# Optimization experiments

Hardware: AMD Instinct MI355X
Metric: run time of the kernel (lower is better)

The kernel has to match this reference:

```python
import jax, jax.numpy as jnp
import numpy as np

BATCH, SEQ, D_MODEL, STATE_DIM = 8, 2048, 1024, 1024


def setup_inputs() -> dict:
    key = jax.random.key(0)
    k1, k2, k3, k4 = jax.random.split(key, 4)
    u = jax.random.normal(k1, (BATCH, SEQ, D_MODEL), dtype=jnp.float32)
    a_params = jax.random.normal(k2, (STATE_DIM // 2,), dtype=jnp.float32) * 0.1
    # nn.Linear default init ~ U(-1/sqrt(fan_in), 1/sqrt(fan_in)); scaled normal is fine for a baseline
    B_w = jax.random.normal(k3, (STATE_DIM, D_MODEL), dtype=jnp.float32) / np.sqrt(D_MODEL).astype(np.float32)
    C_w = jax.random.normal(k4, (D_MODEL, STATE_DIM), dtype=jnp.float32) / np.sqrt(STATE_DIM).astype(np.float32)
    D = jnp.zeros((D_MODEL,), dtype=jnp.float32)
    return {"u": u, "a_params": a_params, "B_w": B_w, "C_w": C_w, "D": D}


def _cayley_circulant_eigenvalues(a_params, n):
    # Build skew-circulant first column: a[0]=0, a[1:n/2]=a_params[:n/2-1], a[n/2]=0,
    # a[n/2+1:] = -flip(a_params[:n/2-1]); eigenvalues are purely imaginary: i*omega.
    half_n = n // 2
    a_full = jnp.zeros((n,), dtype=a_params.dtype)
    a_full = a_full.at[1:half_n].set(a_params[: half_n - 1])
    a_full = a_full.at[half_n + 1 :].set(-a_params[: half_n - 1][::-1])
    omega = jnp.fft.fft(a_full).imag
    # Cayley transform (1 - i*w)/(1 + i*w) = ((1-w^2) - 2iw) / (1+w^2)
    w2 = omega * omega
    denom = 1.0 + w2
    return (((1.0 - w2) / denom) + 1j * (-2.0 * omega / denom)).astype(jnp.complex64)


def reference(u, a_params, B_w, C_w, D):
    n = B_w.shape[0]
    lambdas = _cayley_circulant_eigenvalues(a_params, n)  # (n,) complex64
    Bu = jnp.einsum("bsd,nd->bsn", u, B_w)  # (b, s, n)

    def step(h, bu_t):
        # W h via FFT diagonalization of the circulant W (W real => real part exact)
        Wh = jnp.fft.ifft(lambdas * jnp.fft.fft(h.astype(jnp.float32))).real.astype(h.dtype)
        h_new = Wh + bu_t
        return h_new, h_new

    h0 = jnp.zeros((u.shape[0], n), dtype=u.dtype)
    _, hs = jax.lax.scan(step, h0, jnp.swapaxes(Bu, 0, 1))  # hs: (s, b, n)
    y = jnp.einsum("sbn,dn->bsd", hs, C_w) + D * u  # (b, s, d)
    return y
```

## Files before the change

kernel.cpp:

```cpp
#include <hip/hip_runtime.h>
#include <math.h>

#define BATCH   8
#define SEQLEN  2048
#define DMODEL  1024
#define KFREQ   513
#define NSPEC   1024
#define NPAIR   512
#define BT_ROWS (BATCH*SEQLEN)
#define NC      32
#define TC      64

static_assert(NC * TC == SEQLEN, "chunking must cover SEQLEN");

typedef __attribute__((ext_vector_type(4))) float f32x4;
typedef __attribute__((ext_vector_type(8))) short bf16x8;
typedef unsigned short ushort_t;
typedef unsigned int uint_t;

__device__ __forceinline__ ushort_t f2bf(float f) {
    union { float f; unsigned u; } v; v.f = f;
    unsigned r = v.u + 0x7FFFu + ((v.u >> 16) & 1u);
    return (ushort_t)(r >> 16);
}
__device__ __forceinline__ float bf2f(ushort_t b) {
    union { unsigned u; float f; } v; v.u = ((unsigned)b) << 16;
    return v.f;
}

__device__ __forceinline__ void async_cp16(const void* g, void* l) {
    __builtin_amdgcn_global_load_lds(
        (const __attribute__((address_space(1))) void*)g,
        (__attribute__((address_space(3))) void*)l, 16, 0, 0);
}

#define BAR()   __builtin_amdgcn_s_barrier()
#define PRIO1() __builtin_amdgcn_s_setprio(1)
#define PRIO0() __builtin_amdgcn_s_setprio(0)
#define LGKM0() asm volatile("s_waitcnt lgkmcnt(0)" ::: "memory")
#define LGKM8() asm volatile("s_waitcnt lgkmcnt(8)" ::: "memory")
#define VM6()   asm volatile("s_waitcnt vmcnt(6)" ::: "memory")
#define VM0()   asm volatile("s_waitcnt vmcnt(0)" ::: "memory")

#define SINSTEP 0.00613592315154256491887f

#define NB_T  (NSPEC * DMODEL / 8 / 256)
#define NB_TR 256
#define NB_CW (DMODEL * DMODEL / 8 / 256)
#define NB_U  (BT_ROWS * DMODEL / 8 / 256)

__global__ __launch_bounds__(256) void prep_all(const float* __restrict__ ap,
                                                float* __restrict__ lam,
                                                const float* __restrict__ Dv,
                                                int* __restrict__ dflag,
                                                const float* __restrict__ Cw,
                                                ushort_t* __restrict__ Cwb,
                                                const float* __restrict__ Bw,
                                                ushort_t* __restrict__ BwTb,
                                                ushort_t* __restrict__ T1b,
                                                ushort_t* __restrict__ T2b,
                                                const float* __restrict__ u,
                                                ushort_t* __restrict__ ub) {
    const int bid = blockIdx.x;
    if (bid == 0) {
        __shared__ float stab[1024];
        __shared__ float apl[512];
        __shared__ int anyd;
        if (threadIdx.x == 0) anyd = 0;
        for (int j = threadIdx.x; j < 1024; j += 256)
            stab[j] = sinf((float)j * SINSTEP);
        for (int j = threadIdx.x; j < 511; j += 256)
            apl[j] = ap[j];
        __syncthreads();
        for (int q = threadIdx.x; q < 1024; q += 256)
            if (Dv[q] != 0.0f) anyd = 1;
        for (int f = threadIdx.x; f < KFREQ; f += 256) {
            float o0 = 0.0f, o1 = 0.0f, o2 = 0.0f, o3 = 0.0f;
            int j = 1;
            for (; j + 3 <= 511; j += 4) {
                o0 = fmaf(apl[j - 1], stab[(j * f) & 1023], o0);
                o1 = fmaf(apl[j],     stab[((j + 1) * f) & 1023], o1);
                o2 = fmaf(apl[j + 1], stab[((j + 2) * f) & 1023], o2);
                o3 = fmaf(apl[j + 2], stab[((j + 3) * f) & 1023], o3);
            }
            for (; j <= 511; ++j)
                o0 = fmaf(apl[j - 1], stab[(j * f) & 1023], o0);
            const float om = ((o0 + o1) + (o2 + o3)) * -2.0f;
            const float w2 = om * om;
            const float den = 1.0f + w2;
            const float re = (1.0f - w2) / den;
            const float im = -2.0f * om / den;
            if (f == 0)        lam[0] = re;
            else if (f == 512) lam[1] = re;
            else { lam[2 * f] = re; lam[2 * f + 1] = im; }
        }
        __syncthreads();
        if (threadIdx.x == 0) *dflag = anyd;
    } else if (bid < 1 + 2 * NB_T) {
        __shared__ float stab[1024];
        for (int j = threadIdx.x; j < 1024; j += 256)
            stab[j] = sinf((float)j * SINSTEP);
        __syncthreads();
        const int t = bid - 1;
        const int mode = t >= NB_T;
        ushort_t* T = mode ? T2b : T1b;
        const int i = (t - mode * NB_T) * 256 + threadIdx.x;
        const int row = i >> 7;
        const int nb  = (i & 127) << 3;
        const int kf  = (row == 1) ? 512 : (row >> 1);
        const bool sb = (row & 1) && (row != 1);
        float scale = 1.0f;
        if (mode) scale = ((row < 2) ? 1.0f : 2.0f) / 1024.0f;
        ushort_t o[8];
        int m = (kf * nb) & 1023;
#pragma unroll
        for (int j = 0; j < 8; ++j) {
            const float v = sb ? -stab[m] : stab[(m + 256) & 1023];
            o[j] = f2bf(v * scale);
            m = (m + kf) & 1023;
        }
        reinterpret_cast<bf16x8*>(T)[i] = *reinterpret_cast<bf16x8*>(o);
    } else if (bid < 1 + 2 * NB_T + NB_TR) {
        __shared__ float tile[64][65];
        const int b2 = bid - (1 + 2 * NB_T);
        const int bx = (b2 & 15) * 64;
        const int by = (b2 >> 4) * 64;
        const int lx = threadIdx.x & 63;
        const int ly = threadIdx.x >> 6;
#pragma unroll
        for (int i = 0; i < 16; ++i) {
            const int r = ly + i * 4;
            tile[r][lx] = Bw[(size_t)(by + r) * DMODEL + bx + lx];
        }
        __syncthreads();
#pragma unroll
        for (int i = 0; i < 16; ++i) {
            const int r = ly + i * 4;
            BwTb[(size_t)(bx + r) * DMODEL + by + lx] = f2bf(tile[lx][r]);
        }
    } else if (bid < 1 + 2 * NB_T + NB_TR + NB_CW) {
        const int b3 = bid - (1 + 2 * NB_T + NB_TR);
        const int i = b3 * 256 + threadIdx.x;
        const float4 a = reinterpret_cast<const float4*>(Cw)[2 * i];
        const float4 b = reinterpret_cast<const float4*>(Cw)[2 * i + 1];
        ushort_t o[8] = {f2bf(a.x), f2bf(a.y), f2bf(a.z), f2bf(a.w),
                         f2bf(b.x), f2bf(b.y), f2bf(b.z), f2bf(b.w)};
        reinterpret_cast<bf16x8*>(Cwb)[i] = *reinterpret_cast<bf16x8*>(o);
    } else {
        const int b4 = bid - (1 + 2 * NB_T + NB_TR + NB_CW);
        const int i = b4 * 256 + threadIdx.x;
        const float4 a = reinterpret_cast<const float4*>(u)[2 * i];
        const float4 b = reinterpret_cast<const float4*>(u)[2 * i + 1];
        ushort_t o[8] = {f2bf(a.x), f2bf(a.y), f2bf(a.z), f2bf(a.w),
                         f2bf(b.x), f2bf(b.y), f2bf(b.z), f2bf(b.w)};
        reinterpret_cast<bf16x8*>(ub)[i] = *reinterpret_cast<bf16x8*>(o);
    }
}

__global__ __launch_bounds__(256) void gemm128z(const ushort_t* __restrict__ A0,
                                                const ushort_t* __restrict__ B0,
                                                ushort_t* __restrict__ C0,
                                                const ushort_t* __restrict__ A1,
                                                const ushort_t* __restrict__ B1,
                                                ushort_t* __restrict__ C1) {
    const int K = 1024, N = 1024;
    const ushort_t* A = blockIdx.z ? A1 : A0;
    const ushort_t* B = blockIdx.z ? B1 : B0;
    ushort_t*       C = blockIdx.z ? C1 : C0;
    __shared__ ushort_t As[128 * 32];
    __shared__ ushort_t Bs[128 * 32];
    const int tid  = threadIdx.x;
    const int lane = tid & 63;
    const int w    = tid >> 6;
    const int m0 = blockIdx.x * 128;
    const int n0 = blockIdx.y * 128;
    const int wr = (w >> 1) * 64;
    const int wc = (w & 1) * 64;

    f32x4 acc[4][4] = {};

    const int pos  = w * 512 + lane * 8;
    const int srow = pos >> 5;
    const int scol = pos & 31;
    const int lr = lane & 15;
    const int lk = (lane >> 4) * 8;

    for (int k0 = 0; k0 < K; k0 += 32) {
        __syncthreads();
        async_cp16(A + (size_t)(m0 + srow)      * K + k0 + scol, As + w * 512);
        async_cp16(A + (size_t)(m0 + srow + 64) * K + k0 + scol, As + 2048 + w * 512);
        async_cp16(B + (size_t)(n0 + srow)      * K + k0 + scol, Bs + w * 512);
        async_cp16(B + (size_t)(n0 + srow + 64) * K + k0 + scol, Bs + 2048 + w * 512);
        __syncthreads();

        bf16x8 fa[4], fb[4];
#pragma unroll
        for (int mi = 0; mi < 4; ++mi)
            fa[mi] = *reinterpret_cast<const bf16x8*>(&As[(wr + mi * 16 + lr) * 32 + lk]);
#pragma unroll
        for (int ni = 0; ni < 4; ++ni)
            fb[ni] = *reinterpret_cast<const bf16x8*>(&Bs[(wc + ni * 16 + lr) * 32 + lk]);
#pragma unroll
        for (int mi = 0; mi < 4; ++mi)
#pragma unroll
            for (int ni = 0; ni < 4; ++ni)
                acc[mi][ni] = __builtin_amdgcn_mfma_f32_16x16x32_bf16(
                    fa[mi], fb[ni], acc[mi][ni], 0, 0, 0);
    }

    const int rbase = (lane >> 4) * 4;
#pragma unroll
    for (int mi = 0; mi < 4; ++mi)
#pragma unroll
        for (int ni = 0; ni < 4; ++ni) {
            const int col = n0 + wc + ni * 16 + lr;
#pragma unroll
            for (int j = 0; j < 4; ++j) {
                const int row = m0 + wr + mi * 16 + rbase + j;
                C[(size_t)row * N + col] = f2bf(acc[mi][ni][j]);
            }
        }
}

__device__ __forceinline__ void pair_coef(const float* lam, int j,
                                          float& lr, float& lr2, float& cr) {
    const float a = lam[2 * j];
    const float b = lam[2 * j + 1];
    if (j == 0) { lr = a; lr2 = b; cr = 0.0f; }
    else        { lr = a; lr2 = a; cr = b; }
}

template <int MH, int NH>
__device__ __forceinline__ void quad_mfma(f32x4 (&acc)[2][2][4][2],
                                          const bf16x8 (&fa)[4][2],
                                          const bf16x8 (&fb)[2][2]) {
#pragma unroll
    for (int mi = 0; mi < 4; ++mi)
#pragma unroll
        for (int ni = 0; ni < 2; ++ni) {
            acc[MH][NH][mi][ni] = __builtin_amdgcn_mfma_f32_16x16x32_bf16(
                fa[mi][0], fb[ni][0], acc[MH][NH][mi][ni], 0, 0, 0);
            acc[MH][NH][mi][ni] = __builtin_amdgcn_mfma_f32_16x16x32_bf16(
                fa[mi][1], fb[ni][1], acc[MH][NH][mi][ni], 0, 0, 0);
        }
}

__device__ __forceinline__ void ld_fa(bf16x8 (&fa)[4][2], const ushort_t* hb,
                                      int wm, int lr, int c0, int c1) {
#pragma unroll
    for (int mi = 0; mi < 4; ++mi) {
        const ushort_t* p = hb + (wm * 64 + mi * 16 + lr) * 64;
        fa[mi][0] = *reinterpret_cast<const bf16x8*>(p + c0);
        fa[mi][1] = *reinterpret_cast<const bf16x8*>(p + c1);
    }
}
__device__ __forceinline__ void ld_fb(bf16x8 (&fb)[2][2], const ushort_t* hb,
                                      int wn, int lr, int c0, int c1) {
#pragma unroll
    for (int ni = 0; ni < 2; ++ni) {
        const ushort_t* p = hb + (wn * 32 + ni * 16 + lr) * 64;
        fb[ni][0] = *reinterpret_cast<const bf16x8*>(p + c0);
        fb[ni][1] = *reinterpret_cast<const bf16x8*>(p + c1);
    }
}

#define HS_STRIDE 260

template <bool SCANEPI>
__global__ __launch_bounds__(512, 2) void gemm256(const ushort_t* __restrict__ A,
                                                  const ushort_t* __restrict__ B,
                                                  void* __restrict__ Cv,
                                                  int M, int K,
                                                  const float* __restrict__ uu,
                                                  const float* __restrict__ Dv,
                                                  const int* __restrict__ dflag,
                                                  const float* __restrict__ lam,
                                                  float2* __restrict__ G) {
    __shared__ ushort_t smem[66560];
    const int tid  = threadIdx.x;
    const int lane = tid & 63;
    const int w    = tid >> 6;
    const int wm   = w >> 2;
    const int wn   = w & 3;
    const int m0 = blockIdx.x * 256;
    const int n0 = blockIdx.y * 256;
    const int lr = lane & 15;
    const int lk = (lane >> 4) * 8;
    const int xv = (lr & 7) << 3;
    const int c0 = lk ^ xv;
    const int c1 = (32 + lk) ^ xv;

    const int rA = tid >> 3;
    const int cS = ((tid & 7) << 3) ^ ((rA & 7) << 3);
    const int ldsOff = w << 9;

    auto ApH = [&](int buf, int half) { return smem + (buf * 2 + half) * 8192; };
    auto BpH = [&](int buf, int half) { return smem + 32768 + (buf * 2 + half) * 8192; };

    f32x4 acc[2][2][4][2] = {};
    bf16x8 fa[4][2], fbl[2][2], fbh[2][2];

    auto stA = [&](int buf, int half, int k) {
#pragma unroll
        for (int li = 0; li < 2; ++li)
            async_cp16(A + (size_t)(m0 + half * 128 + li * 64 + rA) * K + k + cS,
                       ApH(buf, half) + li * 4096 + ldsOff);
    };
    auto stB = [&](int buf, int half, int k) {
#pragma unroll
        for (int li = 0; li < 2; ++li)
            async_cp16(B + (size_t)(n0 + half * 128 + li * 64 + rA) * K + k + cS,
                       BpH(buf, half) + li * 4096 + ldsOff);
    };

    stA(0, 0, 0); stB(0, 0, 0); stB(0, 1, 0); stA(0, 1, 0);
    stA(1, 0, 64); stB(1, 0, 64); stB(1, 1, 64);
    VM6();
    BAR();

    const int niter = K >> 7;
#pragma unroll 1
    for (int t = 0; t < niter - 1; ++t) {
        const int kb1 = (t << 7) + 64;
        const int kn  = (t + 1) << 7;
        const int kn2 = kn + 64;
        ld_fa(fa, ApH(0, 0), wm, lr, c0, c1);
        ld_fb(fbl, BpH(0, 0), wn, lr, c0, c1);
        stA(1, 1, kb1);
        LGKM8();
        BAR(); LGKM0();
        PRIO1(); quad_mfma<0, 0>(acc, fa, fbl); PRIO0();
        BAR();
        ld_fb(fbh, BpH(0, 1), wn, lr, c0, c1);
        stA(0, 0, kn);
        BAR(); LGKM0();
        PRIO1(); quad_mfma<0, 1>(acc, fa, fbh); PRIO0();
        BAR();
        ld_fa(fa, ApH(0, 1), wm, lr, c0, c1);
        stB(0, 0, kn);
        BAR(); LGKM0();
        PRIO1(); quad_mfma<1, 1>(acc, fa, fbh); PRIO0();
        BAR();
        stB(0, 1, kn);
        VM6();
        BAR();
        PRIO1(); quad_mfma<1, 0>(acc, fa, fbl); PRIO0();
        BAR();
        ld_fa(fa, ApH(1, 0), wm, lr, c0, c1);
        ld_fb(fbl, BpH(1, 0), wn, lr, c0, c1);
        stA(0, 1, kn);
        LGKM8();
        BAR(); LGKM0();
        PRIO1(); quad_mfma<0, 0>(acc, fa, fbl); PRIO0();
        BAR();
        ld_fb(fbh, BpH(1, 1), wn, lr, c0, c1);
        stA(1, 0, kn2);
        BAR(); LGKM0();
        PRIO1(); quad_mfma<0, 1>(acc, fa, fbh); PRIO0();
        BAR();
        ld_fa(fa, ApH(1, 1), wm, lr, c0, c1);
        stB(1, 0, kn2);
        BAR(); LGKM0();
        PRIO1(); quad_mfma<1, 1>(acc, fa, fbh); PRIO0();
        BAR();
        stB(1, 1, kn2);
        VM6();
        BAR();
        PRIO1(); quad_mfma<1, 0>(acc, fa, fbl); PRIO0();
        BAR();
    }
    {
        const int kb1 = ((niter - 1) << 7) + 64;
        ld_fa(fa, ApH(0, 0), wm, lr, c0, c1);
        ld_fb(fbl, BpH(0, 0), wn, lr, c0, c1);
        stA(1, 1, kb1);
        LGKM8();
        BAR(); LGKM0();
        PRIO1(); quad_mfma<0, 0>(acc, fa, fbl); PRIO0();
        BAR();
        ld_fb(fbh, BpH(0, 1), wn, lr, c0, c1);
        BAR(); LGKM0();
        PRIO1(); quad_mfma<0, 1>(acc, fa, fbh); PRIO0();
        BAR();
        ld_fa(fa, ApH(0, 1), wm, lr, c0, c1);
        BAR(); LGKM0();
        PRIO1(); quad_mfma<1, 1>(acc, fa, fbh); PRIO0();
        BAR();
        VM0();
        BAR();
        PRIO1(); quad_mfma<1, 0>(acc, fa, fbl); PRIO0();
        BAR();
        ld_fa(fa, ApH(1, 0), wm, lr, c0, c1);
        ld_fb(fbl, BpH(1, 0), wn, lr, c0, c1);
        BAR(); LGKM0();
        PRIO1(); quad_mfma<0, 0>(acc, fa, fbl); PRIO0();
        BAR();
        ld_fb(fbh, BpH(1, 1), wn, lr, c0, c1);
        BAR(); LGKM0();
        PRIO1(); quad_mfma<0, 1>(acc, fa, fbh); PRIO0();
        BAR();
        ld_fa(fa, ApH(1, 1), wm, lr, c0, c1);
        BAR(); LGKM0();
        PRIO1(); quad_mfma<1, 1>(acc, fa, fbh); PRIO0();
        BAR();
        PRIO1(); quad_mfma<1, 0>(acc, fa, fbl); PRIO0();
    }

    const int rbase = (lane >> 4) * 4;
    if (SCANEPI) {
        BAR();
#pragma unroll
        for (int mh = 0; mh < 2; ++mh)
#pragma unroll
            for (int nh = 0; nh < 2; ++nh)
#pragma unroll
                for (int mi = 0; mi < 4; ++mi)
#pragma unroll
                    for (int ni = 0; ni < 2; ++ni) {
                        const int cl = nh * 128 + wn * 32 + ni * 16 + lr;
#pragma unroll
                        for (int j = 0; j < 4; ++j) {
                            const int rl = mh * 128 + wm * 64 + mi * 16 + rbase + j;
                            smem[rl * HS_STRIDE + cl] = f2bf(acc[mh][nh][mi][ni][j]);
                        }
                    }
        BAR();
        const int chunk = tid >> 7;
        const int p = tid & 127;
        const int jg = (n0 >> 1) + p;
        float lr_, lr2_, cr_;
        pair_coef(lam, jg, lr_, lr2_, cr_);
        uint_t* gout = reinterpret_cast<uint_t*>((ushort_t*)Cv +
                        (size_t)(m0 + chunk * TC) * NSPEC) + jg;
        float er = 0.0f, ei = 0.0f;
        for (int t = 0; t < TC; ++t) {
            const uint_t v = *reinterpret_cast<const uint_t*>(
                &smem[(chunk * TC + t) * HS_STRIDE + 2 * p]);
            const float ur = bf2f((ushort_t)(v & 0xFFFF));
            const float ui = bf2f((ushort_t)(v >> 16));
            const float nr = fmaf(lr_, er, fmaf(-cr_, ei, ur));
            const float ni = fmaf(lr2_, ei, fmaf(cr_, er, ui));
            gout[(size_t)t * NPAIR] = (uint_t)f2bf(nr) | ((uint_t)f2bf(ni) << 16);
            er = nr; ei = ni;
        }
        const int b = m0 >> 11;
        const int cg = ((m0 & 2047) >> 6) + chunk;
        G[(size_t)(b * NC + cg) * NPAIR + jg] = make_float2(er, ei);
    } else {
        float* C = (float*)Cv;
        const bool du = (*dflag != 0);
#pragma unroll
        for (int mh = 0; mh < 2; ++mh)
#pragma unroll
            for (int nh = 0; nh < 2; ++nh)
#pragma unroll
                for (int mi = 0; mi < 4; ++mi)
#pragma unroll
                    for (int ni = 0; ni < 2; ++ni) {
                        const int col = n0 + nh * 128 + wn * 32 + ni * 16 + lr;
#pragma unroll
                        for (int j = 0; j < 4; ++j) {
                            const int row = m0 + mh * 128 + wm * 64 + mi * 16 + rbase + j;
                            float v = acc[mh][nh][mi][ni][j];
                            if (du) v = fmaf(Dv[col], uu[(size_t)row * DMODEL + col], v);
                            C[(size_t)row * DMODEL + col] = v;
                        }
                    }
    }
}

__global__ __launch_bounds__(256) void scan_applyc(ushort_t* __restrict__ UHb,
                                                   const float* __restrict__ lam,
                                                   const float2* __restrict__ G) {
    const int gid = blockIdx.x * 256 + threadIdx.x;
    const int j = gid & (NPAIR - 1);
    const int s9 = gid >> 9;
    const int c = 1 + s9 % 31;
    const int b = s9 / 31;
    float lr, lr2, cr;
    pair_coef(lam, j, lr, lr2, cr);
    float pr = lr, pr2 = lr2, pc = cr;
    for (int s = 0; s < 6; ++s) {
        const float nr  = pr * pr - pc * pc;
        const float nr2 = pr2 * pr2 - pc * pc;
        const float npc = pc * (pr + pr2);
        pr = nr; pr2 = nr2; pc = npc;
    }
    float er = 0.0f, ei = 0.0f;
    for (int cp = 0; cp < c; ++cp) {
        const float2 g = G[(size_t)(b * NC + cp) * NPAIR + j];
        const float nr = fmaf(pr, er, fmaf(-pc, ei, g.x));
        const float ni = fmaf(pr2, ei, fmaf(pc, er, g.y));
        er = nr; ei = ni;
    }
    float sr = fmaf(lr, er, -cr * ei);
    float si = fmaf(lr2, ei, cr * er);
    uint_t* base = reinterpret_cast<uint_t*>(
        UHb + (size_t)(b * SEQLEN + c * TC) * NSPEC) + j;
    for (int t = 0; t < TC; ++t) {
        const uint_t v = base[(size_t)t * NPAIR];
        const float hr = bf2f((ushort_t)(v & 0xFFFF)) + sr;
        const float hi = bf2f((ushort_t)(v >> 16)) + si;
        base[(size_t)t * NPAIR] = (uint_t)f2bf(hr) | ((uint_t)f2bf(hi) << 16);
        const float nsr = fmaf(lr, sr, -cr * si);
        const float nsi = fmaf(lr2, si, cr * sr);
        sr = nsr; si = nsi;
    }
}

extern "C" void kernel_launch(void* const* d_in, const int* in_sizes, int n_in,
                              void* d_out, int out_size, void* d_ws, size_t ws_size,
                              hipStream_t stream) {
    const float* u  = (const float*)d_in[0];
    const float* ap = (const float*)d_in[1];
    const float* Bw = (const float*)d_in[2];
    const float* Cw = (const float*)d_in[3];
    const float* Dv = (const float*)d_in[4];
    float* out = (float*)d_out;

    char* ws = (char*)d_ws;
    size_t off = 0;
    auto carve = [&](size_t bytes) { char* p = ws + off; off += (bytes + 255) & ~(size_t)255; return p; };

    ushort_t* UHb  = (ushort_t*)carve((size_t)BT_ROWS * NSPEC * sizeof(ushort_t));
    ushort_t* ub   = (ushort_t*)carve((size_t)BT_ROWS * DMODEL * sizeof(ushort_t));
    ushort_t* T1b  = (ushort_t*)carve((size_t)NSPEC * DMODEL * sizeof(ushort_t));
    ushort_t* T2b  = (ushort_t*)carve((size_t)NSPEC * DMODEL * sizeof(ushort_t));
    ushort_t* BwTb = (ushort_t*)carve((size_t)DMODEL * DMODEL * sizeof(ushort_t));
    ushort_t* Cwb  = (ushort_t*)carve((size_t)DMODEL * DMODEL * sizeof(ushort_t));
    ushort_t* W1b  = (ushort_t*)carve((size_t)NSPEC * DMODEL * sizeof(ushort_t));
    ushort_t* W2b  = (ushort_t*)carve((size_t)DMODEL * NSPEC * sizeof(ushort_t));
    float*    lam  = (float*)   carve(NSPEC * sizeof(float));
    int*      dflag= (int*)     carve(sizeof(int));
    float2*   G    = (float2*)  carve((size_t)BATCH * NC * NPAIR * sizeof(float2));

    prep_all<<<1 + 2 * NB_T + NB_TR + NB_CW + NB_U, 256, 0, stream>>>(
        ap, lam, Dv, dflag, Cw, Cwb, Bw, BwTb, T1b, T2b, u, ub);

    {
        dim3 g(8, 8, 2);
        gemm128z<<<g, 256, 0, stream>>>(T1b, BwTb, W1b, Cwb, T2b, W2b);
    }

    {
        dim3 g(BT_ROWS / 256, NSPEC / 256);
        gemm256<true><<<g, 512, 0, stream>>>(ub, W1b, UHb,
            BT_ROWS, DMODEL, nullptr, nullptr, dflag, lam, G);
    }

    scan_applyc<<<BATCH * 31 * NPAIR / 256, 256, 0, stream>>>(UHb, lam, G);

    {
        dim3 g(BT_ROWS / 256, DMODEL / 256);
        gemm256<false><<<g, 512, 0, stream>>>(UHb, W2b, out,
            BT_ROWS, NSPEC, u, Dv, dflag, lam, nullptr);
    }
}
```

Before: 145.5 us.

## Fuse chunk-carry scan into first GEMM epilogue via grid-wide atomic barrier

Drops the separate scan_applyc kernel. The first GEMM now keeps its chunk-local scan results in LDS, publishes chunk carries to G, and waits at a grid-wide atomic counter barrier. It then combines the prefix carries and writes the corrected hidden states to global memory once, instead of writing them and later reading and rewriting them. The gain is one fewer launch and one fewer read-modify-write pass over UHb. The risk is deadlock if the 64x4=256 blocks are not all resident at once (2 per CU, 256 CUs), plus some idle time while blocks spin.

```diff
diff --git a/kernel.cpp b/kernel.cpp
--- a/kernel.cpp
+++ b/kernel.cpp
@@ -60,13 +60,14 @@
                                                 ushort_t* __restrict__ T1b,
                                                 ushort_t* __restrict__ T2b,
                                                 const float* __restrict__ u,
-                                                ushort_t* __restrict__ ub) {
+                                                ushort_t* __restrict__ ub,
+                                                uint_t* __restrict__ cnt) {
     const int bid = blockIdx.x;
     if (bid == 0) {
         __shared__ float stab[1024];
         __shared__ float apl[512];
         __shared__ int anyd;
-        if (threadIdx.x == 0) anyd = 0;
+        if (threadIdx.x == 0) { anyd = 0; *cnt = 0; }
         for (int j = threadIdx.x; j < 1024; j += 256)
             stab[j] = sinf((float)j * SINSTEP);
         for (int j = threadIdx.x; j < 511; j += 256)
@@ -275,7 +276,8 @@
                                                   const float* __restrict__ Dv,
                                                   const int* __restrict__ dflag,
                                                   const float* __restrict__ lam,
-                                                  float2* __restrict__ G) {
+                                                  float2* __restrict__ G,
+                                                  uint_t* __restrict__ cnt) {
     __shared__ ushort_t smem[66560];
     const int tid  = threadIdx.x;
     const int lane = tid & 63;
@@ -430,22 +432,65 @@
         const int jg = (n0 >> 1) + p;
         float lr_, lr2_, cr_;
         pair_coef(lam, jg, lr_, lr2_, cr_);
-        uint_t* gout = reinterpret_cast<uint_t*>((ushort_t*)Cv +
-                        (size_t)(m0 + chunk * TC) * NSPEC) + jg;
-        float er = 0.0f, ei = 0.0f;
-        for (int t = 0; t < TC; ++t) {
-            const uint_t v = *reinterpret_cast<const uint_t*>(
-                &smem[(chunk * TC + t) * HS_STRIDE + 2 * p]);
-            const float ur = bf2f((ushort_t)(v & 0xFFFF));
-            const float ui = bf2f((ushort_t)(v >> 16));
-            const float nr = fmaf(lr_, er, fmaf(-cr_, ei, ur));
-            const float ni = fmaf(lr2_, ei, fmaf(cr_, er, ui));
-            gout[(size_t)t * NPAIR] = (uint_t)f2bf(nr) | ((uint_t)f2bf(ni) << 16);
-            er = nr; ei = ni;
-        }
-        const int b = m0 >> 11;
-        const int cg = ((m0 & 2047) >> 6) + chunk;
-        G[(size_t)(b * NC + cg) * NPAIR + jg] = make_float2(er, ei);
+        uint_t* hs = reinterpret_cast<uint_t*>(smem);
+        {
+            float er = 0.0f, ei = 0.0f;
+            for (int t = 0; t < TC; ++t) {
+                const int off = (chunk * TC + t) * (HS_STRIDE / 2) + p;
+                const uint_t v = hs[off];
+                const float ur = bf2f((ushort_t)(v & 0xFFFF));
+                const float ui = bf2f((ushort_t)(v >> 16));
+                const float nr = fmaf(lr_, er, fmaf(-cr_, ei, ur));
+                const float ni = fmaf(lr2_, ei, fmaf(cr_, er, ui));
+                hs[off] = (uint_t)f2bf(nr) | ((uint_t)f2bf(ni) << 16);
+                er = nr; ei = ni;
+            }
+            const int b = m0 >> 11;
+            const int cg = ((m0 & 2047) >> 6) + chunk;
+            G[(size_t)(b * NC + cg) * NPAIR + jg] = make_float2(er, ei);
+        }
+        __threadfence();
+        __syncthreads();
+        if (tid == 0) {
+            const uint_t target = gridDim.x * gridDim.y;
+            __hip_atomic_fetch_add(cnt, 1u, __ATOMIC_RELEASE,
+                                   __HIP_MEMORY_SCOPE_AGENT);
+            while (__hip_atomic_load(cnt, __ATOMIC_ACQUIRE,
+                                     __HIP_MEMORY_SCOPE_AGENT) < target) {}
+        }
+        __syncthreads();
+        __threadfence();
+        {
+            const int b = m0 >> 11;
+            const int cg = ((m0 & 2047) >> 6) + chunk;
+            float pr = lr_, pr2 = lr2_, pc = cr_;
+            for (int s = 0; s < 6; ++s) {
+                const float nr  = pr * pr - pc * pc;
+                const float nr2 = pr2 * pr2 - pc * pc;
+                const float npc = pc * (pr + pr2);
+                pr = nr; pr2 = nr2; pc = npc;
+            }
+            float er = 0.0f, ei = 0.0f;
+            for (int cp = 0; cp < cg; ++cp) {
+                const float2 g = G[(size_t)(b * NC + cp) * NPAIR + jg];
+                const float nr = fmaf(pr, er, fmaf(-pc, ei, g.x));
+                const float ni = fmaf(pr2, ei, fmaf(pc, er, g.y));
+                er = nr; ei = ni;
+            }
+            float sr = fmaf(lr_, er, -cr_ * ei);
+            float si = fmaf(lr2_, ei, cr_ * er);
+            uint_t* gout = reinterpret_cast<uint_t*>((ushort_t*)Cv +
+                            (size_t)(m0 + chunk * TC) * NSPEC) + jg;
+            for (int t = 0; t < TC; ++t) {
+                const uint_t v = hs[(chunk * TC + t) * (HS_STRIDE / 2) + p];
+                const float hr = bf2f((ushort_t)(v & 0xFFFF)) + sr;
+                const float hi = bf2f((ushort_t)(v >> 16)) + si;
+                gout[(size_t)t * NPAIR] = (uint_t)f2bf(hr) | ((uint_t)f2bf(hi) << 16);
+                const float nsr = fmaf(lr_, sr, -cr_ * si);
+                const float nsi = fmaf(lr2_, si, cr_ * sr);
+                sr = nsr; si = nsi;
+            }
+        }
     } else {
         float* C = (float*)Cv;
         const bool du = (*dflag != 0);
@@ -466,45 +511,6 @@
                             C[(size_t)row * DMODEL + col] = v;
                         }
                     }
-    }
-}
-
-__global__ __launch_bounds__(256) void scan_applyc(ushort_t* __restrict__ UHb,
-                                                   const float* __restrict__ lam,
-                                                   const float2* __restrict__ G) {
-    const int gid = blockIdx.x * 256 + threadIdx.x;
-    const int j = gid & (NPAIR - 1);
-    const int s9 = gid >> 9;
-    const int c = 1 + s9 % 31;
-    const int b = s9 / 31;
-    float lr, lr2, cr;
-    pair_coef(lam, j, lr, lr2, cr);
-    float pr = lr, pr2 = lr2, pc = cr;
-    for (int s = 0; s < 6; ++s) {
-        const float nr  = pr * pr - pc * pc;
-        const float nr2 = pr2 * pr2 - pc * pc;
-        const float npc = pc * (pr + pr2);
-        pr = nr; pr2 = nr2; pc = npc;
-    }
-    float er = 0.0f, ei = 0.0f;
-    for (int cp = 0; cp < c; ++cp) {
-        const float2 g = G[(size_t)(b * NC + cp) * NPAIR + j];
-        const float nr = fmaf(pr, er, fmaf(-pc, ei, g.x));
-        const float ni = fmaf(pr2, ei, fmaf(pc, er, g.y));
-        er = nr; ei = ni;
-    }
-    float sr = fmaf(lr, er, -cr * ei);
-    float si = fmaf(lr2, ei, cr * er);
-    uint_t* base = reinterpret_cast<uint_t*>(
-        UHb + (size_t)(b * SEQLEN + c * TC) * NSPEC) + j;
-    for (int t = 0; t < TC; ++t) {
-        const uint_t v = base[(size_t)t * NPAIR];
-        const float hr = bf2f((ushort_t)(v & 0xFFFF)) + sr;
-        const float hi = bf2f((ushort_t)(v >> 16)) + si;
-        base[(size_t)t * NPAIR] = (uint_t)f2bf(hr) | ((uint_t)f2bf(hi) << 16);
-        const float nsr = fmaf(lr, sr, -cr * si);
-        const float nsi = fmaf(lr2, si, cr * sr);
-        sr = nsr; si = nsi;
     }
 }
 
@@ -532,10 +538,11 @@
     ushort_t* W2b  = (ushort_t*)carve((size_t)DMODEL * NSPEC * sizeof(ushort_t));
     float*    lam  = (float*)   carve(NSPEC * sizeof(float));
     int*      dflag= (int*)     carve(sizeof(int));
+    uint_t*   cnt  = (uint_t*)  carve(sizeof(uint_t));
     float2*   G    = (float2*)  carve((size_t)BATCH * NC * NPAIR * sizeof(float2));
 
     prep_all<<<1 + 2 * NB_T + NB_TR + NB_CW + NB_U, 256, 0, stream>>>(
-        ap, lam, Dv, dflag, Cw, Cwb, Bw, BwTb, T1b, T2b, u, ub);
+        ap, lam, Dv, dflag, Cw, Cwb, Bw, BwTb, T1b, T2b, u, ub, cnt);
 
     {
         dim3 g(8, 8, 2);
@@ -545,14 +552,12 @@
     {
         dim3 g(BT_ROWS / 256, NSPEC / 256);
         gemm256<true><<<g, 512, 0, stream>>>(ub, W1b, UHb,
-            BT_ROWS, DMODEL, nullptr, nullptr, dflag, lam, G);
-    }
-
-    scan_applyc<<<BATCH * 31 * NPAIR / 256, 256, 0, stream>>>(UHb, lam, G);
+            BT_ROWS, DMODEL, nullptr, nullptr, dflag, lam, G, cnt);
+    }
 
     {
         dim3 g(BT_ROWS / 256, DMODEL / 256);
         gemm256<false><<<g, 512, 0, stream>>>(UHb, W2b, out,
-            BT_ROWS, NSPEC, u, Dv, dflag, lam, nullptr);
-    }
-}
+            BT_ROWS, NSPEC, u, Dv, dflag, lam, nullptr, cnt);
+    }
+}
```

New measurement: 212.6 us. 1.46x slower.
